# Kernel optimization log

Hardware: AMD Instinct MI355X
Metric: run time of the kernel (lower is better)

Reference implementation:

```python
import jax, jax.numpy as jnp
import numpy as np

NCE_T = 0.07   # opt.nce_T
EPS = 1e-8     # torch CosineSimilarity eps
DIAG_FILL = -10.0

N, D = 8192, 256

def setup_inputs() -> dict:
    key = jax.random.key(0)
    kq, kk = jax.random.split(key)
    feat_q = jax.random.normal(kq, (N, D), dtype=jnp.float32)
    feat_k = jax.random.normal(kk, (N, D), dtype=jnp.float32)
    return {"feat_q": feat_q, "feat_k": feat_k}

def reference(feat_q, feat_k):
    # feat_k is detached in the original
    feat_k = jax.lax.stop_gradient(feat_k)
    nq = jnp.linalg.norm(feat_q, axis=-1)            # [N]
    nk = jnp.linalg.norm(feat_k, axis=-1)            # [N]
    # positive cosine similarity (paired rows)
    l_pos = jnp.sum(feat_q * feat_k, axis=-1) / jnp.maximum(nq * nk, EPS)  # [N]
    # full N x N cosine similarity via GEMM (torch does a broadcasted version)
    sim = (feat_q @ feat_k.T) / jnp.maximum(nq[:, None] * nk[None, :], EPS)  # [N,N]
    # mask self-similarities with -10.0 BEFORE dividing by temperature
    diag = jnp.eye(sim.shape[0], dtype=bool)
    l_neg = jnp.where(diag, DIAG_FILL, sim)
    out = jnp.concatenate([l_pos[:, None], l_neg], axis=1) / NCE_T  # [N, N+1]
    # cross-entropy vs target class 0, reduction='none'
    loss = jax.scipy.special.logsumexp(out, axis=1) - out[:, 0]     # [N]
    return loss
```

## Files before the change

kernel.cpp:

```cpp
#include <hip/hip_runtime.h>
#include <stdint.h>
#include <math.h>

#define NROWS 8192
#define DDIM  256
#define BM    128
#define BN    128
#define GJ    8
#define COLS_PER_GROUP (NROWS / GJ)

constexpr float INV_T  = 1.0f / 0.07f;
constexpr float LOG2E  = 1.44269504f;
constexpr float K1     = INV_T * LOG2E;

typedef __bf16 bf16x8 __attribute__((ext_vector_type(8)));
typedef float  f32x4  __attribute__((ext_vector_type(4)));

__device__ __forceinline__ void async_copy16(const uint16_t* g, uint16_t* l) {
    __builtin_amdgcn_global_load_lds(
        (const __attribute__((address_space(1))) uint32_t*)g,
        (__attribute__((address_space(3))) uint32_t*)l, 16, 0, 0);
}

__device__ inline uint16_t f2bf(float f) {
    uint32_t u = __float_as_uint(f);
    u += 0x7fffu + ((u >> 16) & 1u);
    return (uint16_t)(u >> 16);
}

__global__ __launch_bounds__(256) void norm_convert_kernel(
    const float* __restrict__ fq, const float* __restrict__ fk,
    uint16_t* __restrict__ qb, uint16_t* __restrict__ kb,
    float* __restrict__ lpT)
{
    const int wave = threadIdx.x >> 6;
    const int lane = threadIdx.x & 63;
    const int row  = blockIdx.x * 4 + wave;

    if (row < NROWS) {
        const float* qsrc = fq + (size_t)row * DDIM;
        const float* ksrc = fk + (size_t)row * DDIM;
        float4 vq = ((const float4*)qsrc)[lane];
        float4 vk = ((const float4*)ksrc)[lane];
        float ssq = vq.x*vq.x + vq.y*vq.y + vq.z*vq.z + vq.w*vq.w;
        float ssk = vk.x*vk.x + vk.y*vk.y + vk.z*vk.z + vk.w*vk.w;
        float dqk = vq.x*vk.x + vq.y*vk.y + vq.z*vk.z + vq.w*vk.w;
        #pragma unroll
        for (int m = 1; m < 64; m <<= 1) {
            ssq += __shfl_xor(ssq, m, 64);
            ssk += __shfl_xor(ssk, m, 64);
            dqk += __shfl_xor(dqk, m, 64);
        }
        float r = rsqrtf(ssq);
        ushort4 o;
        o.x = f2bf(vq.x * r); o.y = f2bf(vq.y * r); o.z = f2bf(vq.z * r); o.w = f2bf(vq.w * r);
        ((ushort4*)(qb + (size_t)row * DDIM))[lane] = o;
        if (lane == 0) {
            float denom = fmaxf(sqrtf(ssq) * sqrtf(ssk), 1e-8f);
            lpT[row] = (dqk / denom) * INV_T;
        }
    } else {
        const int r_ = row - NROWS;
        const float* src = fk + (size_t)r_ * DDIM;
        float4 v = ((const float4*)src)[lane];
        float ss = v.x*v.x + v.y*v.y + v.z*v.z + v.w*v.w;
        #pragma unroll
        for (int m = 1; m < 64; m <<= 1) ss += __shfl_xor(ss, m, 64);
        float r = rsqrtf(ss);
        ushort4 o;
        o.x = f2bf(v.x * r); o.y = f2bf(v.y * r); o.z = f2bf(v.z * r); o.w = f2bf(v.w * r);
        ((ushort4*)(kb + (size_t)r_ * DDIM))[lane] = o;
    }
}

__global__ __launch_bounds__(256, 2) void nce_main_kernel(
    const uint16_t* __restrict__ qb, const uint16_t* __restrict__ kb,
    float* __restrict__ gpl)
{
    __shared__ __align__(16) uint16_t lds_q[BM * DDIM];
    __shared__ __align__(16) uint16_t lds_k[8192];

    const int tid    = threadIdx.x;
    const int wave   = tid >> 6;
    const int lane   = tid & 63;
    const int quad   = lane >> 4;
    const int lanelo = lane & 15;
    const int rowBase      = blockIdx.x * BM;
    const int colGroupBase = blockIdx.y * COLS_PER_GROUP;

    #pragma unroll
    for (int i = 0; i < 16; ++i) {
        int S   = (wave * 16 + i) * 64 + lane;
        int row = S >> 5;
        int ch  = (S & 31) ^ (row & 31);
        async_copy16(qb + (size_t)(rowBase + row) * DDIM + ch * 8,
                     lds_q + (size_t)(wave * 16 + i) * 512);
    }

    const int c0 = (lane & 3) ^ ((lane >> 3) & 3);
    const uint16_t* kpb0 = kb + (size_t)(colGroupBase + wave * 32 +      (lane >> 2)) * DDIM + c0 * 8;
    const uint16_t* kpb1 = kb + (size_t)(colGroupBase + wave * 32 + 16 + (lane >> 2)) * DDIM + c0 * 8;
    uint16_t* kw = lds_k + wave * 2048;

    async_copy16(kpb0,      kw);
    async_copy16(kpb1,      kw + 512);
    async_copy16(kpb0 + 32, kw + 1024);
    async_copy16(kpb1 + 32, kw + 1536);

    __syncthreads();

    int bvoff[2];
    #pragma unroll
    for (int nt = 0; nt < 2; ++nt)
        bvoff[nt] = (nt * 16 + lanelo) * 32 + (quad ^ ((lanelo >> 1) & 3)) * 8;

    float l_run[32];
    #pragma unroll
    for (int i = 0; i < 32; ++i) l_run[i] = 0.f;

    for (int jt = 0; jt < 8; ++jt) {
        f32x4 acc[8][2];
        #pragma unroll
        for (int mt = 0; mt < 8; ++mt)
            #pragma unroll
            for (int nt = 0; nt < 2; ++nt)
                acc[mt][nt] = (f32x4){0.f, 0.f, 0.f, 0.f};

        #pragma unroll
        for (int kk = 0; kk < 8; ++kk) {
            const int p = (jt << 3) + kk;

            asm volatile("s_waitcnt vmcnt(2)" ::: "memory");

            bf16x8 av[8], bv[2];
            #pragma unroll
            for (int mt = 0; mt < 8; ++mt) {
                int rq  = mt * 16 + lanelo;
                int chp = ((kk << 2) + quad) ^ (lanelo + ((mt & 1) << 4));
                av[mt] = *(const bf16x8*)&lds_q[rq * 256 + chp * 8];
            }
            const int bufo = (p & 1) << 10;
            bv[0] = *(const bf16x8*)&lds_k[wave * 2048 + bufo + bvoff[0]];
            bv[1] = *(const bf16x8*)&lds_k[wave * 2048 + bufo + bvoff[1]];

            asm volatile("s_waitcnt lgkmcnt(0)" ::: "memory");
            {
                const int np  = (p + 2) & 63;
                const int off = ((np >> 3) << 15) + ((np & 7) << 5);
                async_copy16(kpb0 + off, kw + bufo);
                async_copy16(kpb1 + off, kw + bufo + 512);
            }
            __builtin_amdgcn_sched_barrier(0);

            #pragma unroll
            for (int mt = 0; mt < 8; ++mt)
                #pragma unroll
                for (int nt = 0; nt < 2; ++nt)
                    acc[mt][nt] = __builtin_amdgcn_mfma_f32_16x16x32_bf16(
                        av[mt], bv[nt], acc[mt][nt], 0, 0, 0);
        }

        #pragma unroll
        for (int mt = 0; mt < 8; ++mt) {
            #pragma unroll
            for (int rg = 0; rg < 4; ++rg) {
                float s = exp2f(fmaf(acc[mt][0][rg], K1, -K1))
                        + exp2f(fmaf(acc[mt][1][rg], K1, -K1));
                l_run[mt * 4 + rg] += s;
            }
        }
    }

    #pragma unroll
    for (int i = 0; i < 32; ++i) {
        float v = l_run[i];
        v += __shfl_xor(v, 1, 64);
        v += __shfl_xor(v, 2, 64);
        v += __shfl_xor(v, 4, 64);
        v += __shfl_xor(v, 8, 64);
        l_run[i] = v;
    }

    __syncthreads();

    float* pl = (float*)lds_k;
    if (lanelo == 0) {
        #pragma unroll
        for (int mt = 0; mt < 8; ++mt)
            #pragma unroll
            for (int rg = 0; rg < 4; ++rg)
                pl[wave * 128 + mt * 16 + quad * 4 + rg] = l_run[mt * 4 + rg];
    }
    __syncthreads();
    if (tid < 128) {
        float L = pl[tid] + pl[128 + tid] + pl[256 + tid] + pl[384 + tid];
        gpl[(size_t)blockIdx.y * NROWS + rowBase + tid] = L;
    }
}

__global__ __launch_bounds__(256) void finalize_kernel(
    const float* __restrict__ gpl, const float* __restrict__ lpT,
    float* __restrict__ out)
{
    int t = blockIdx.x * 256 + threadIdx.x;
    if (t >= NROWS) return;
    float L = 0.f;
    #pragma unroll
    for (int g = 0; g < GJ; ++g) L += gpl[g * NROWS + t];
    out[t] = INV_T + __logf(L) - lpT[t];
}

extern "C" void kernel_launch(void* const* d_in, const int* in_sizes, int n_in,
                              void* d_out, int out_size, void* d_ws, size_t ws_size,
                              hipStream_t stream) {
    const float* fq = (const float*)d_in[0];
    const float* fk = (const float*)d_in[1];
    char* ws = (char*)d_ws;
    uint16_t* qb  = (uint16_t*)(ws);
    uint16_t* kb  = (uint16_t*)(ws + 4194304);
    float*    lpT = (float*)(ws + 8388608);
    float*    gpl = (float*)(ws + 8421376);

    norm_convert_kernel<<<(2 * NROWS) / 4, 256, 0, stream>>>(fq, fk, qb, kb, lpT);
    dim3 grid(NROWS / BM, GJ);
    nce_main_kernel<<<grid, 256, 0, stream>>>(qb, kb, gpl);
    finalize_kernel<<<NROWS / 256, 256, 0, stream>>>(gpl, lpT, (float*)d_out);
}
```

Before: 105.6 us.

## Use two waves per block with 64-column wave tiles in main GEMM kernel

Each main-kernel block now runs 2 waves instead of 4. Each wave covers 64 key columns per step (4 MFMA n-tiles) instead of 32, so every A fragment read from LDS feeds twice as many MFMAs. The double-buffered K staging and the async copy counts are resized to match. The cost is a larger accumulator and register footprint per wave and fewer waves per block to hide latency, which may lower occupancy.

```diff
diff --git a/kernel.cpp b/kernel.cpp
--- a/kernel.cpp
+++ b/kernel.cpp
@@ -73,12 +73,12 @@
     }
 }
 
-__global__ __launch_bounds__(256, 2) void nce_main_kernel(
+__global__ __launch_bounds__(128, 1) void nce_main_kernel(
     const uint16_t* __restrict__ qb, const uint16_t* __restrict__ kb,
     float* __restrict__ gpl)
 {
     __shared__ __align__(16) uint16_t lds_q[BM * DDIM];
-    __shared__ __align__(16) uint16_t lds_k[8192];
+    __shared__ __align__(16) uint16_t lds_k[2 * 2 * 2048];
 
     const int tid    = threadIdx.x;
     const int wave   = tid >> 6;
@@ -89,29 +89,30 @@
     const int colGroupBase = blockIdx.y * COLS_PER_GROUP;
 
     #pragma unroll
-    for (int i = 0; i < 16; ++i) {
-        int S   = (wave * 16 + i) * 64 + lane;
+    for (int i = 0; i < 32; ++i) {
+        int S   = (wave * 32 + i) * 64 + lane;
         int row = S >> 5;
         int ch  = (S & 31) ^ (row & 31);
         async_copy16(qb + (size_t)(rowBase + row) * DDIM + ch * 8,
-                     lds_q + (size_t)(wave * 16 + i) * 512);
+                     lds_q + (size_t)(wave * 32 + i) * 512);
     }
 
     const int c0 = (lane & 3) ^ ((lane >> 3) & 3);
-    const uint16_t* kpb0 = kb + (size_t)(colGroupBase + wave * 32 +      (lane >> 2)) * DDIM + c0 * 8;
-    const uint16_t* kpb1 = kb + (size_t)(colGroupBase + wave * 32 + 16 + (lane >> 2)) * DDIM + c0 * 8;
-    uint16_t* kw = lds_k + wave * 2048;
-
-    async_copy16(kpb0,      kw);
-    async_copy16(kpb1,      kw + 512);
-    async_copy16(kpb0 + 32, kw + 1024);
-    async_copy16(kpb1 + 32, kw + 1536);
+    const uint16_t* kb_r =
+        kb + (size_t)(colGroupBase + wave * 64 + (lane >> 2)) * DDIM + c0 * 8;
+    uint16_t* kw = lds_k + wave * 4096;
+
+    #pragma unroll
+    for (int b = 0; b < 2; ++b)
+        #pragma unroll
+        for (int j = 0; j < 4; ++j)
+            async_copy16(kb_r + j * 4096 + b * 32, kw + b * 2048 + j * 512);
 
     __syncthreads();
 
-    int bvoff[2];
-    #pragma unroll
-    for (int nt = 0; nt < 2; ++nt)
+    int bvoff[4];
+    #pragma unroll
+    for (int nt = 0; nt < 4; ++nt)
         bvoff[nt] = (nt * 16 + lanelo) * 32 + (quad ^ ((lanelo >> 1) & 3)) * 8;
 
     float l_run[32];
@@ -119,43 +120,45 @@
     for (int i = 0; i < 32; ++i) l_run[i] = 0.f;
 
     for (int jt = 0; jt < 8; ++jt) {
-        f32x4 acc[8][2];
+        f32x4 acc[8][4];
         #pragma unroll
         for (int mt = 0; mt < 8; ++mt)
             #pragma unroll
-            for (int nt = 0; nt < 2; ++nt)
+            for (int nt = 0; nt < 4; ++nt)
                 acc[mt][nt] = (f32x4){0.f, 0.f, 0.f, 0.f};
 
         #pragma unroll
         for (int kk = 0; kk < 8; ++kk) {
             const int p = (jt << 3) + kk;
 
-            asm volatile("s_waitcnt vmcnt(2)" ::: "memory");
-
-            bf16x8 av[8], bv[2];
+            asm volatile("s_waitcnt vmcnt(4)" ::: "memory");
+
+            bf16x8 av[8], bv[4];
             #pragma unroll
             for (int mt = 0; mt < 8; ++mt) {
                 int rq  = mt * 16 + lanelo;
                 int chp = ((kk << 2) + quad) ^ (lanelo + ((mt & 1) << 4));
                 av[mt] = *(const bf16x8*)&lds_q[rq * 256 + chp * 8];
             }
-            const int bufo = (p & 1) << 10;
-            bv[0] = *(const bf16x8*)&lds_k[wave * 2048 + bufo + bvoff[0]];
-            bv[1] = *(const bf16x8*)&lds_k[wave * 2048 + bufo + bvoff[1]];
+            const int bufo = (p & 1) << 11;
+            #pragma unroll
+            for (int nt = 0; nt < 4; ++nt)
+                bv[nt] = *(const bf16x8*)&lds_k[wave * 4096 + bufo + bvoff[nt]];
 
             asm volatile("s_waitcnt lgkmcnt(0)" ::: "memory");
             {
                 const int np  = (p + 2) & 63;
                 const int off = ((np >> 3) << 15) + ((np & 7) << 5);
-                async_copy16(kpb0 + off, kw + bufo);
-                async_copy16(kpb1 + off, kw + bufo + 512);
+                #pragma unroll
+                for (int j = 0; j < 4; ++j)
+                    async_copy16(kb_r + j * 4096 + off, kw + bufo + j * 512);
             }
             __builtin_amdgcn_sched_barrier(0);
 
             #pragma unroll
             for (int mt = 0; mt < 8; ++mt)
                 #pragma unroll
-                for (int nt = 0; nt < 2; ++nt)
+                for (int nt = 0; nt < 4; ++nt)
                     acc[mt][nt] = __builtin_amdgcn_mfma_f32_16x16x32_bf16(
                         av[mt], bv[nt], acc[mt][nt], 0, 0, 0);
         }
@@ -164,8 +167,10 @@
         for (int mt = 0; mt < 8; ++mt) {
             #pragma unroll
             for (int rg = 0; rg < 4; ++rg) {
-                float s = exp2f(fmaf(acc[mt][0][rg], K1, -K1))
-                        + exp2f(fmaf(acc[mt][1][rg], K1, -K1));
+                float s = 0.f;
+                #pragma unroll
+                for (int nt = 0; nt < 4; ++nt)
+                    s += exp2f(fmaf(acc[mt][nt][rg], K1, -K1));
                 l_run[mt * 4 + rg] += s;
             }
         }
@@ -193,7 +198,7 @@
     }
     __syncthreads();
     if (tid < 128) {
-        float L = pl[tid] + pl[128 + tid] + pl[256 + tid] + pl[384 + tid];
+        float L = pl[tid] + pl[128 + tid];
         gpl[(size_t)blockIdx.y * NROWS + rowBase + tid] = L;
     }
 }
@@ -223,6 +228,6 @@
 
     norm_convert_kernel<<<(2 * NROWS) / 4, 256, 0, stream>>>(fq, fk, qb, kb, lpT);
     dim3 grid(NROWS / BM, GJ);
-    nce_main_kernel<<<grid, 256, 0, stream>>>(qb, kb, gpl);
+    nce_main_kernel<<<grid, 128, 0, stream>>>(qb, kb, gpl);
     finalize_kernel<<<NROWS / 256, 256, 0, stream>>>(gpl, lpT, (float*)d_out);
 }
```

New measurement: 110.8 us. 1.05x slower.
